# Kernel tuning notes

Measured on AMD Instinct MI355X. Metric: run time of the kernel, lower is better.

## Reference

```python
import jax, jax.numpy as jnp
import numpy as np

VOCAB = 32000
DIM = 256
PAD = 0
EPS = 1e-12


def setup_inputs() -> dict:
    key = jax.random.key(0)
    k1, k2, k3 = jax.random.split(key, 3)
    input_ids = jax.random.randint(k1, (32, 128, 32), 0, VOCAB)
    table = jax.random.normal(k2, (VOCAB, DIM), dtype=jnp.float32) * 0.02
    table = table.at[PAD].set(0.0)  # padding_idx row is zero
    gamma = jnp.ones((DIM,), dtype=jnp.float32)
    beta = jnp.zeros((DIM,), dtype=jnp.float32)
    return {"input_ids": input_ids, "table": table, "gamma": gamma, "beta": beta}


def reference(input_ids, table, gamma, beta):
    # gather: [B, S, W, D]
    emb = table[input_ids]
    mu = jnp.mean(emb, axis=-1, keepdims=True)
    var = jnp.mean(jnp.square(emb - mu), axis=-1, keepdims=True)
    normed = (emb - mu) * jax.lax.rsqrt(var + EPS) * gamma + beta
    # dropout is identity in eval mode; SentenceMethod.SUM reduces over words (dim=2)
    return normed.sum(axis=2)  # [B, S, D]
```

## Files before the change

### kernel.cpp

```cpp
#include <hip/hip_runtime.h>

#define N_ROWS 4096
#define W      32
#define DIM    256
#define TE_EPS 1e-12f

__global__ __launch_bounds__(256) void te_kernel(
    const int*   __restrict__ ids,
    const float* __restrict__ table,
    const float* __restrict__ gamma,
    const float* __restrict__ beta,
    float*       __restrict__ out)
{
    const int wave = (blockIdx.x * blockDim.x + threadIdx.x) >> 6;
    const int lane = threadIdx.x & 63;

    const float4 g = *reinterpret_cast<const float4*>(gamma + lane * 4);
    const float4 b = *reinterpret_cast<const float4*>(beta  + lane * 4);

    const int myidx = ids[wave * W + (lane & 31)];

    float4 acc = make_float4(0.f, 0.f, 0.f, 0.f);

    #pragma unroll 4
    for (int w = 0; w < W; ++w) {
        const int id = __shfl(myidx, w);
        const float4 v = *reinterpret_cast<const float4*>(
            table + (size_t)id * DIM + lane * 4);

        float s  = v.x + v.y + v.z + v.w;
        float sq = v.x * v.x + v.y * v.y + v.z * v.z + v.w * v.w;
        #pragma unroll
        for (int off = 32; off > 0; off >>= 1) {
            s  += __shfl_xor(s,  off);
            sq += __shfl_xor(sq, off);
        }
        const float mu  = s * (1.0f / 256.0f);
        const float var = sq * (1.0f / 256.0f) - mu * mu;
        const float rs  = rsqrtf(var + TE_EPS);

        acc.x += (v.x - mu) * rs;
        acc.y += (v.y - mu) * rs;
        acc.z += (v.z - mu) * rs;
        acc.w += (v.w - mu) * rs;
    }

    float4 o;
    o.x = acc.x * g.x + (float)W * b.x;
    o.y = acc.y * g.y + (float)W * b.y;
    o.z = acc.z * g.z + (float)W * b.z;
    o.w = acc.w * g.w + (float)W * b.w;

    *reinterpret_cast<float4*>(out + (size_t)wave * DIM + lane * 4) = o;
}

extern "C" void kernel_launch(void* const* d_in, const int* in_sizes, int n_in,
                              void* d_out, int out_size, void* d_ws, size_t ws_size,
                              hipStream_t stream) {
    const int*   ids   = (const int*)  d_in[0];
    const float* table = (const float*)d_in[1];
    const float* gamma = (const float*)d_in[2];
    const float* beta  = (const float*)d_in[3];
    float*       out   = (float*)      d_out;

    te_kernel<<<N_ROWS / 4, 256, 0, stream>>>(ids, table, gamma, beta, out);
}
```

Measured before the change: 101.1 us.

## Split each output row's 32-word sum across four waves with LDS reduction

Each block now handles one output row, and each of its four waves gathers and normalizes 8 of the 32 word embeddings instead of one wave doing all 32. Partial sums are combined through shared memory after a barrier, and wave 0 applies gamma/beta and writes the result. The goal is four times more independent waves with a shorter dependent gather chain each, so more table loads are in flight to hide memory latency. In exchange it adds a block barrier, an LDS round trip, and four times as many blocks.

```diff
diff --git a/kernel.cpp b/kernel.cpp
--- a/kernel.cpp
+++ b/kernel.cpp
@@ -12,18 +12,19 @@
     const float* __restrict__ beta,
     float*       __restrict__ out)
 {
-    const int wave = (blockIdx.x * blockDim.x + threadIdx.x) >> 6;
-    const int lane = threadIdx.x & 63;
+    const int row  = blockIdx.x;
+    const int tid  = threadIdx.x;
+    const int wv   = tid >> 6;
+    const int lane = tid & 63;
 
-    const float4 g = *reinterpret_cast<const float4*>(gamma + lane * 4);
-    const float4 b = *reinterpret_cast<const float4*>(beta  + lane * 4);
+    __shared__ float4 part[3][64];
 
-    const int myidx = ids[wave * W + (lane & 31)];
+    const int myidx = ids[row * W + wv * 8 + (lane & 7)];
 
     float4 acc = make_float4(0.f, 0.f, 0.f, 0.f);
 
-    #pragma unroll 4
-    for (int w = 0; w < W; ++w) {
+    #pragma unroll
+    for (int w = 0; w < 8; ++w) {
         const int id = __shfl(myidx, w);
         const float4 v = *reinterpret_cast<const float4*>(
             table + (size_t)id * DIM + lane * 4);
@@ -45,13 +46,31 @@
         acc.w += (v.w - mu) * rs;
     }
 
-    float4 o;
-    o.x = acc.x * g.x + (float)W * b.x;
-    o.y = acc.y * g.y + (float)W * b.y;
-    o.z = acc.z * g.z + (float)W * b.z;
-    o.w = acc.w * g.w + (float)W * b.w;
+    if (wv != 0) {
+        part[wv - 1][lane] = acc;
+    }
+    __syncthreads();
 
-    *reinterpret_cast<float4*>(out + (size_t)wave * DIM + lane * 4) = o;
+    if (wv == 0) {
+        const float4 a1 = part[0][lane];
+        const float4 a2 = part[1][lane];
+        const float4 a3 = part[2][lane];
+        acc.x += a1.x + a2.x + a3.x;
+        acc.y += a1.y + a2.y + a3.y;
+        acc.z += a1.z + a2.z + a3.z;
+        acc.w += a1.w + a2.w + a3.w;
+
+        const float4 g = *reinterpret_cast<const float4*>(gamma + lane * 4);
+        const float4 b = *reinterpret_cast<const float4*>(beta  + lane * 4);
+
+        float4 o;
+        o.x = acc.x * g.x + (float)W * b.x;
+        o.y = acc.y * g.y + (float)W * b.y;
+        o.z = acc.z * g.z + (float)W * b.z;
+        o.w = acc.w * g.w + (float)W * b.w;
+
+        *reinterpret_cast<float4*>(out + (size_t)row * DIM + lane * 4) = o;
+    }
 }
 
 extern "C" void kernel_launch(void* const* d_in, const int* in_sizes, int n_in,
@@ -63,5 +82,5 @@
     const float* beta  = (const float*)d_in[3];
     float*       out   = (float*)      d_out;
 
-    te_kernel<<<N_ROWS / 4, 256, 0, stream>>>(ids, table, gamma, beta, out);
+    te_kernel<<<N_ROWS, 256, 0, stream>>>(ids, table, gamma, beta, out);
 }
```

Result: faster. 97.00 us (-4.1%).
